# Optimization experiments

Hardware: AMD Instinct MI355X
Metric: run time of the kernel (lower is better)

The kernel has to match this reference:

```python
import jax, jax.numpy as jnp
import numpy as np

B, L, D_TOK, N_HEAD, D_QK, D_V, TOPK = 4, 1024, 897, 8, 512, 768, 8
NEG = -10000.0


def setup_inputs() -> dict:
    key = jax.random.key(0)
    ks = jax.random.split(key, 8)
    q = jax.random.normal(ks[0], (B, L, D_TOK), jnp.float32)
    k = jax.random.normal(ks[1], (B, L, D_TOK), jnp.float32)
    v = jax.random.normal(ks[2], (B, L, D_V), jnp.float32)
    # self-patch exclusion mask (registered buffer 10000*eye, applied negatively)
    qk_mask = NEG * jnp.eye(L, dtype=jnp.float32)[None, None]  # [1,1,L,L]
    k_mask = jax.random.normal(ks[3], (B, 1, L, 1), jnp.float32)  # additive key mask
    w_qs = jax.random.normal(ks[4], (D_TOK, N_HEAD * D_QK), jnp.float32) / np.sqrt(D_TOK)
    w_ks = jax.random.normal(ks[5], (D_TOK, N_HEAD * D_QK), jnp.float32) / np.sqrt(D_TOK)
    w_vs = jax.random.normal(ks[6], (D_V, N_HEAD * D_V), jnp.float32) / np.sqrt(D_V)
    w_fc = jax.random.normal(ks[7], (N_HEAD * D_V, D_V), jnp.float32) / np.sqrt(N_HEAD * D_V)
    return {"q": q, "k": k, "v": v, "qk_mask": qk_mask, "k_mask": k_mask,
            "w_qs": w_qs, "w_ks": w_ks, "w_vs": w_vs, "w_fc": w_fc}


def _topk_sparsify(attn):
    # keep top-k scores per query row, set the rest to -10000 (exact torch scatter semantics)
    vals, idx = jax.lax.top_k(attn, TOPK)                      # [B,H,L,TOPK]
    flat = jnp.full((B * N_HEAD * L, L), NEG, attn.dtype)
    rows = jnp.arange(B * N_HEAD * L)[:, None]
    flat = flat.at[rows, idx.reshape(-1, TOPK)].set(vals.reshape(-1, TOPK))
    return flat.reshape(B, N_HEAD, L, L)


def reference(q, k, v, qk_mask, k_mask, w_qs, w_ks, w_vs, w_fc):
    # projections -> [B, H, L, d]
    qh = (q @ w_qs).reshape(B, L, N_HEAD, D_QK).transpose(0, 2, 1, 3)
    kh = (k @ w_ks).reshape(B, L, N_HEAD, D_QK).transpose(0, 2, 1, 3)
    vh = (v @ w_vs).reshape(B, L, N_HEAD, D_V).transpose(0, 2, 1, 3)
    scale = 1.0 / jnp.sqrt(jnp.asarray(D_QK, qh.dtype))
    attn = jnp.einsum('bhqd,bhkd->bhqk', qh * scale, kh)
    attn = attn + qk_mask + k_mask[..., 0][:, :, None, :]      # k_mask.squeeze(-1).unsqueeze(-2)
    attn = _topk_sparsify(attn)
    attn = jax.nn.softmax(attn.astype(jnp.float32), axis=-1).astype(v.dtype)
    out = jnp.einsum('bhqk,bhkd->bhqd', attn, vh)              # [B,H,L,d_v]
    out = out.transpose(0, 2, 1, 3).reshape(B, L, N_HEAD * D_V)
    out = out @ w_fc                                           # [B,L,d_v]; add_residual=False, dropout eval
    return out, attn
```

## Files before the change

### kernel.cpp

```cpp
#include <hip/hip_runtime.h>
#include <math.h>

#define NB 4
#define NL 1024
#define NDT 897
#define NH 8
#define NDQ 512
#define NDV 768
#define NTOP 8
#define NCAND 16
#define KP 928
#define SCALE 0.044194173824159216

typedef unsigned short ushort_t;
typedef __attribute__((ext_vector_type(8))) short short8;
typedef __attribute__((ext_vector_type(4))) float f32x4;

static __device__ __forceinline__ ushort_t f2bf(float f) {
    unsigned u = __float_as_uint(f);
    unsigned r = (u + 0x7fffu + ((u >> 16) & 1u)) >> 16;
    return (ushort_t)r;
}
static __device__ __forceinline__ float bf2f(ushort_t u) {
    return __uint_as_float((unsigned)u << 16);
}
static __device__ __forceinline__ void split3(float x, ushort_t& b1, ushort_t& b2, ushort_t& b3) {
    b1 = f2bf(x);
    float r1 = x - bf2f(b1);
    b2 = f2bf(r1);
    float r2 = r1 - bf2f(b2);
    b3 = f2bf(r2);
}
static __device__ __forceinline__ void split2(float x, ushort_t& b1, ushort_t& b2) {
    b1 = f2bf(x);
    b2 = f2bf(x - bf2f(b1));
}

__global__ __launch_bounds__(256)
void split_w(const float* __restrict__ w_qs, const float* __restrict__ w_ks,
             ushort_t* __restrict__ wsp)
{
    const float* W = (blockIdx.z == 0) ? w_qs : w_ks;
    ushort_t* dst = wsp + (size_t)blockIdx.z * 3 * 4096 * KP;
    const int n0 = blockIdx.x * 64;
    const int k0 = blockIdx.y * 32;
    __shared__ float tf[32][65];
    const int t = threadIdx.x;
#pragma unroll
    for (int it = 0; it < 8; it++) {
        int kk = it * 4 + (t >> 6);
        int nn = t & 63;
        int kg = k0 + kk;
        tf[kk][nn] = (kg < NDT) ? W[(size_t)kg * 4096 + n0 + nn] : 0.f;
    }
    __syncthreads();
    const int nn = t >> 2;
    const int oct = t & 3;
    ushort_t o[3][8];
#pragma unroll
    for (int j = 0; j < 8; j++) {
        float x = tf[oct * 8 + j][nn];
        split3(x, o[0][j], o[1][j], o[2][j]);
    }
#pragma unroll
    for (int p = 0; p < 3; p++)
        *(uint4*)(dst + ((size_t)p * 4096 + n0 + nn) * KP + k0 + oct * 8) = *(const uint4*)o[p];
}

__global__ __launch_bounds__(256)
void split_wvs(const float* __restrict__ w_vs, ushort_t* __restrict__ wvs2)
{
    int gid8 = ((int)blockIdx.x * 256 + threadIdx.x) * 8;
    int dk  = gid8 / 6144;
    int rem = gid8 % 6144;
    int h   = rem / 768;
    int kk  = rem % 768;
    const float* src = w_vs + (size_t)dk * 6144 + rem;
    ushort_t o[2][8];
#pragma unroll
    for (int j = 0; j < 8; j++) split2(src[j], o[0][j], o[1][j]);
#pragma unroll
    for (int p = 0; p < 2; p++)
        *(uint4*)(wvs2 + ((size_t)(p * 8 + h) * 768 + dk) * 768 + kk) = *(const uint4*)o[p];
}

__global__ __launch_bounds__(256)
void split_wfcT(const float* __restrict__ w_fc, ushort_t* __restrict__ wfcT2)
{
    const int dv0 = blockIdx.x * 64;
    const int kg0 = blockIdx.y * 32;
    __shared__ float tf[32][65];
    const int t = threadIdx.x;
#pragma unroll
    for (int it = 0; it < 8; it++) {
        int kk = it * 4 + (t >> 6);
        int dd = t & 63;
        tf[kk][dd] = w_fc[(size_t)(kg0 + kk) * 768 + dv0 + dd];
    }
    __syncthreads();
    const int dv = t >> 2;
    const int oct = t & 3;
    const int h  = kg0 / 768;
    const int kl = kg0 % 768;
    ushort_t o[2][8];
#pragma unroll
    for (int j = 0; j < 8; j++) split2(tf[oct * 8 + j][dv], o[0][j], o[1][j]);
#pragma unroll
    for (int p = 0; p < 2; p++)
        *(uint4*)(wfcT2 + ((size_t)(p * 8 + h) * 768 + dv0 + dv) * 768 + kl + oct * 8) = *(const uint4*)o[p];
}

__global__ __launch_bounds__(256)
void combine_mfma(const ushort_t* __restrict__ wfcT2, const ushort_t* __restrict__ wvs2,
                  ushort_t* __restrict__ MhTb)
{
    const int h = blockIdx.z;
    const int n0 = blockIdx.x * 128, m0 = blockIdx.y * 128;
    __shared__ ushort_t Al[2 * 5120];
    __shared__ ushort_t Bl[2 * 5120];
    const int t = threadIdx.x;
    const int lane = t & 63, wv = t >> 6;
    const int quad = lane >> 4, l16 = lane & 15;

    f32x4 acc[2][8];
#pragma unroll
    for (int i = 0; i < 2; i++)
#pragma unroll
        for (int j = 0; j < 8; j++) acc[i][j] = (f32x4){0.f, 0.f, 0.f, 0.f};

    for (int kc = 0; kc < 768; kc += 32) {
#pragma unroll
        for (int p = 0; p < 2; p++) {
            const ushort_t* Ap = wfcT2 + (size_t)(p * 8 + h) * 768 * 768;
            const ushort_t* Bp = wvs2  + (size_t)(p * 8 + h) * 768 * 768;
#pragma unroll
            for (int pp = 0; pp < 2; pp++) {
                int c = t + pp * 256;
                int r = c >> 2, ck = c & 3;
                int pc = (ck + ((r + (r >> 3)) & 3)) & 3;
                uint4 va = *(const uint4*)(Ap + (size_t)(m0 + r) * 768 + kc + ck * 8);
                *(uint4*)&Al[p * 5120 + r * 40 + pc * 8] = va;
                uint4 vb = *(const uint4*)(Bp + (size_t)(n0 + r) * 768 + kc + ck * 8);
                *(uint4*)&Bl[p * 5120 + r * 40 + pc * 8] = vb;
            }
        }
        __syncthreads();

        short8 af[2][2], bf[2][8];
#pragma unroll
        for (int p = 0; p < 2; p++) {
#pragma unroll
            for (int i = 0; i < 2; i++) {
                int r = wv * 32 + i * 16 + l16;
                int pc = (quad + ((r + (r >> 3)) & 3)) & 3;
                af[p][i] = *(const short8*)&Al[p * 5120 + r * 40 + pc * 8];
            }
#pragma unroll
            for (int j = 0; j < 8; j++) {
                int r = j * 16 + l16;
                int pc = (quad + ((r + (r >> 3)) & 3)) & 3;
                bf[p][j] = *(const short8*)&Bl[p * 5120 + r * 40 + pc * 8];
            }
        }
#pragma unroll
        for (int i = 0; i < 2; i++)
#pragma unroll
            for (int j = 0; j < 8; j++) {
                acc[i][j] = __builtin_amdgcn_mfma_f32_16x16x32_bf16(af[0][i], bf[0][j], acc[i][j], 0, 0, 0);
                acc[i][j] = __builtin_amdgcn_mfma_f32_16x16x32_bf16(af[0][i], bf[1][j], acc[i][j], 0, 0, 0);
                acc[i][j] = __builtin_amdgcn_mfma_f32_16x16x32_bf16(af[1][i], bf[0][j], acc[i][j], 0, 0, 0);
            }
        __syncthreads();
    }

#pragma unroll
    for (int i = 0; i < 2; i++)
#pragma unroll
        for (int j = 0; j < 8; j++) {
            int gn = n0 + j * 16 + l16;
#pragma unroll
            for (int reg = 0; reg < 4; reg++) {
                int gm = m0 + wv * 32 + i * 16 + quad * 4 + reg;
                MhTb[((size_t)h * NDV + gm) * NDV + gn] = f2bf(acc[i][j][reg]);
            }
        }
}

__global__ __launch_bounds__(256)
void split_a(const float* __restrict__ q, const float* __restrict__ k,
             ushort_t* __restrict__ asp, int b)
{
    const int row = blockIdx.x;
    const int z = blockIdx.y;
    const float* A = (z == 0 ? q : k) + ((size_t)b * NL + row) * NDT;
    ushort_t* dst = asp + (size_t)z * 3 * 1024 * KP;
    const int t = threadIdx.x;
    if (t >= 232) return;
    const int kb = t * 4;
    ushort_t o[3][4];
#pragma unroll
    for (int j = 0; j < 4; j++) {
        int kk = kb + j;
        float x = (kk < NDT) ? A[kk] : 0.f;
        split3(x, o[0][j], o[1][j], o[2][j]);
    }
#pragma unroll
    for (int p = 0; p < 3; p++)
        *(uint2*)(dst + ((size_t)p * 1024 + row) * KP + kb) = *(const uint2*)o[p];
}

__global__ __launch_bounds__(256)
void proj_qk_mfma6(const ushort_t* __restrict__ asp, const ushort_t* __restrict__ wsp,
                   float* __restrict__ qh32, float* __restrict__ kh32,
                   ushort_t* __restrict__ qhb, ushort_t* __restrict__ khb)
{
    const int z = blockIdx.z;
    const int n0 = blockIdx.x * 128, m0 = blockIdx.y * 128;
    float*    C32 = z == 0 ? qh32 : kh32;
    ushort_t* Cb  = z == 0 ? qhb  : khb;
    const ushort_t* Ab = asp + (size_t)z * 3 * 1024 * KP;
    const ushort_t* Bb = wsp + (size_t)z * 3 * 4096 * KP;

    __shared__ ushort_t Al[3 * 128 * 40];
    __shared__ ushort_t Bl[3 * 128 * 40];
    const int t = threadIdx.x;
    const int lane = t & 63, wv = t >> 6;
    const int quad = lane >> 4, l16 = lane & 15;

    f32x4 acc[2][8];
#pragma unroll
    for (int i = 0; i < 2; i++)
#pragma unroll
        for (int j = 0; j < 8; j++) acc[i][j] = (f32x4){0.f, 0.f, 0.f, 0.f};

    for (int kc = 0; kc < KP; kc += 32) {
#pragma unroll
        for (int p = 0; p < 3; p++) {
            const ushort_t* Ap = Ab + (size_t)p * 1024 * KP;
            const ushort_t* Bp = Bb + (size_t)p * 4096 * KP;
#pragma unroll
            for (int pp = 0; pp < 2; pp++) {
                int c = t + pp * 256;
                int r = c >> 2, ck = c & 3;
                int pc = (ck + ((r + (r >> 3)) & 3)) & 3;
                uint4 va = *(const uint4*)(Ap + (size_t)(m0 + r) * KP + kc + ck * 8);
                *(uint4*)&Al[p * 5120 + r * 40 + pc * 8] = va;
                uint4 vb = *(const uint4*)(Bp + (size_t)(n0 + r) * KP + kc + ck * 8);
                *(uint4*)&Bl[p * 5120 + r * 40 + pc * 8] = vb;
            }
        }
        __syncthreads();

        short8 af[3][2], bf[3][8];
#pragma unroll
        for (int p = 0; p < 3; p++) {
#pragma unroll
            for (int i = 0; i < 2; i++) {
                int r = wv * 32 + i * 16 + l16;
                int pc = (quad + ((r + (r >> 3)) & 3)) & 3;
                af[p][i] = *(const short8*)&Al[p * 5120 + r * 40 + pc * 8];
            }
#pragma unroll
            for (int j = 0; j < 8; j++) {
                int r = j * 16 + l16;
                int pc = (quad + ((r + (r >> 3)) & 3)) & 3;
                bf[p][j] = *(const short8*)&Bl[p * 5120 + r * 40 + pc * 8];
            }
        }
#pragma unroll
        for (int i = 0; i < 2; i++)
#pragma unroll
            for (int j = 0; j < 8; j++) {
                acc[i][j] = __builtin_amdgcn_mfma_f32_16x16x32_bf16(af[0][i], bf[0][j], acc[i][j], 0, 0, 0);
                acc[i][j] = __builtin_amdgcn_mfma_f32_16x16x32_bf16(af[0][i], bf[1][j], acc[i][j], 0, 0, 0);
                acc[i][j] = __builtin_amdgcn_mfma_f32_16x16x32_bf16(af[1][i], bf[0][j], acc[i][j], 0, 0, 0);
                acc[i][j] = __builtin_amdgcn_mfma_f32_16x16x32_bf16(af[0][i], bf[2][j], acc[i][j], 0, 0, 0);
                acc[i][j] = __builtin_amdgcn_mfma_f32_16x16x32_bf16(af[1][i], bf[1][j], acc[i][j], 0, 0, 0);
                acc[i][j] = __builtin_amdgcn_mfma_f32_16x16x32_bf16(af[2][i], bf[0][j], acc[i][j], 0, 0, 0);
            }
        __syncthreads();
    }

#pragma unroll
    for (int i = 0; i < 2; i++)
#pragma unroll
        for (int j = 0; j < 8; j++) {
            int gn = n0 + j * 16 + l16;
#pragma unroll
            for (int reg = 0; reg < 4; reg++) {
                int gm = m0 + wv * 32 + i * 16 + quad * 4 + reg;
                float vv = acc[i][j][reg];
                C32[(size_t)gm * 4096 + gn] = vv;
                Cb[(size_t)gm * 4096 + gn] = f2bf(vv);
            }
        }
}

__global__ __launch_bounds__(256)
void scores_mfma(const ushort_t* __restrict__ qhb, const ushort_t* __restrict__ khb,
                 const float* __restrict__ kmask, float* __restrict__ sc, int b)
{
    const int h = blockIdx.z;
    const int n0 = blockIdx.x * 128, m0 = blockIdx.y * 128;
    __shared__ ushort_t Al[128 * 40];
    __shared__ ushort_t Bl[128 * 40];
    const int t = threadIdx.x;
    const int lane = t & 63, wv = t >> 6;
    const int quad = lane >> 4, l16 = lane & 15;

    f32x4 acc[2][8];
#pragma unroll
    for (int i = 0; i < 2; i++)
#pragma unroll
        for (int j = 0; j < 8; j++) acc[i][j] = (f32x4){0.f, 0.f, 0.f, 0.f};

    const ushort_t* Ag = qhb + (size_t)h * NDQ;
    const ushort_t* Bg = khb + (size_t)h * NDQ;

    for (int kc = 0; kc < NDQ; kc += 32) {
#pragma unroll
        for (int p = 0; p < 2; p++) {
            int c = t + p * 256;
            int r = c >> 2, ck = c & 3;
            int pc = (ck + ((r + (r >> 3)) & 3)) & 3;
            uint4 va = *(const uint4*)(Ag + (size_t)(m0 + r) * 4096 + kc + ck * 8);
            *(uint4*)&Al[r * 40 + pc * 8] = va;
        }
#pragma unroll
        for (int p = 0; p < 2; p++) {
            int c = t + p * 256;
            int r = c >> 2, ck = c & 3;
            int pc = (ck + ((r + (r >> 3)) & 3)) & 3;
            uint4 vb = *(const uint4*)(Bg + (size_t)(n0 + r) * 4096 + kc + ck * 8);
            *(uint4*)&Bl[r * 40 + pc * 8] = vb;
        }
        __syncthreads();

        short8 af[2], bf[8];
#pragma unroll
        for (int i = 0; i < 2; i++) {
            int r = wv * 32 + i * 16 + l16;
            int pc = (quad + ((r + (r >> 3)) & 3)) & 3;
            af[i] = *(const short8*)&Al[r * 40 + pc * 8];
        }
#pragma unroll
        for (int j = 0; j < 8; j++) {
            int r = j * 16 + l16;
            int pc = (quad + ((r + (r >> 3)) & 3)) & 3;
            bf[j] = *(const short8*)&Bl[r * 40 + pc * 8];
        }
#pragma unroll
        for (int i = 0; i < 2; i++)
#pragma unroll
            for (int j = 0; j < 8; j++)
                acc[i][j] = __builtin_amdgcn_mfma_f32_16x16x32_bf16(af[i], bf[j], acc[i][j], 0, 0, 0);
        __syncthreads();
    }

    const float scl = (float)SCALE;
#pragma unroll
    for (int i = 0; i < 2; i++) {
#pragma unroll
        for (int j = 0; j < 8; j++) {
            int gn = n0 + j * 16 + l16;
            float km = kmask[b * NL + gn];
#pragma unroll
            for (int reg = 0; reg < 4; reg++) {
                int gm = m0 + wv * 32 + i * 16 + quad * 4 + reg;
                float s = acc[i][j][reg] * scl + km;
                if (gm == gn) s -= 10000.0f;
                sc[((size_t)h * NL + gm) * NL + gn] = s;
            }
        }
    }
}

__global__ __launch_bounds__(256)
void select_rescore(float* __restrict__ sc,
                    const float* __restrict__ qh32, const float* __restrict__ kh32,
                    const float* __restrict__ kmask,
                    float* __restrict__ topw, int* __restrict__ topi, int b)
{
    const int lane = threadIdx.x & 63;
    const int w = threadIdx.x >> 6;
    const int r = blockIdx.x * 4 + w;
    const int q = r & 1023, h = r >> 10;

    float* row = sc + (size_t)r * NL;
    float v[16];
#pragma unroll
    for (int j = 0; j < 16; j++) v[j] = row[lane + 64 * j];

    {
        float4 z = make_float4(0.f, 0.f, 0.f, 0.f);
#pragma unroll
        for (int p = 0; p < 4; p++)
            *(float4*)(row + p * 256 + lane * 4) = z;
    }

    int cidx[NCAND];
    for (int tsel = 0; tsel < NCAND; tsel++) {
        float bv = v[0]; int bj = 0;
#pragma unroll
        for (int j = 1; j < 16; j++)
            if (v[j] > bv) { bv = v[j]; bj = j; }
        int bi = lane + 64 * bj;
#pragma unroll
        for (int s = 1; s < 64; s <<= 1) {
            float ov = __shfl_xor(bv, s);
            int   oi = __shfl_xor(bi, s);
            if (ov > bv || (ov == bv && oi < bi)) { bv = ov; bi = oi; }
        }
        cidx[tsel] = bi;
        bool own = (lane == (bi & 63));
        int jj = bi >> 6;
#pragma unroll
        for (int j = 0; j < 16; j++)
            if (own && j == jj) v[j] = -3.0e38f;
    }

    const float* qrow  = qh32 + (size_t)q * 4096 + h * NDQ;
    const float* kbase = kh32 + h * NDQ;
    double qd[8];
#pragma unroll
    for (int j = 0; j < 8; j++) qd[j] = (double)qrow[lane + 64 * j];

    double sv[NCAND]; int si[NCAND];
#pragma unroll
    for (int c = 0; c < NCAND; c++) {
        int idx = cidx[c];
        const float* krow = kbase + (size_t)idx * 4096;
        double s = 0.0;
#pragma unroll
        for (int j = 0; j < 8; j++) s = fma(qd[j], (double)krow[lane + 64 * j], s);
#pragma unroll
        for (int sh = 1; sh < 64; sh <<= 1) s += __shfl_xor(s, sh);
        s = s * SCALE + (double)kmask[b * NL + idx];
        if (idx == q) s -= 10000.0;
        sv[c] = s; si[c] = idx;
    }
    double vs[NTOP]; int is_[NTOP];
    unsigned used = 0;
#pragma unroll
    for (int tsel = 0; tsel < NTOP; tsel++) {
        double bv = -1.0e300; int bi = 1 << 30; int bc = 0;
#pragma unroll
        for (int c = 0; c < NCAND; c++) {
            bool free_c = !(used & (1u << c));
            bool better = free_c && (sv[c] > bv || (sv[c] == bv && si[c] < bi));
            if (better) { bv = sv[c]; bi = si[c]; bc = c; }
        }
        used |= (1u << bc);
        vs[tsel] = bv; is_[tsel] = bi;
    }
    double m = vs[0];
    double e[NTOP], Z = 0.0;
#pragma unroll
    for (int i = 0; i < NTOP; i++) { e[i] = exp(vs[i] - m); Z += e[i]; }

    __asm__ volatile("s_waitcnt vmcnt(0)" ::: "memory");

    if (lane == 0) {
#pragma unroll
        for (int i = 0; i < NTOP; i++) {
            float wv = (float)(e[i] / Z);
            topw[(size_t)r * NTOP + i] = wv;
            topi[(size_t)r * NTOP + i] = is_[i];
            row[is_[i]] = wv;
        }
    }
}

__global__ __launch_bounds__(256)
void conv_v_bf16(const float* __restrict__ v, ushort_t* __restrict__ vb)
{
    size_t i = ((size_t)blockIdx.x * 256 + threadIdx.x) * 4;
    float4 f = *(const float4*)(v + i);
    ushort_t o[4] = { f2bf(f.x), f2bf(f.y), f2bf(f.z), f2bf(f.w) };
    *(uint2*)(vb + i) = *(uint2*)o;
}

__global__ __launch_bounds__(256)
void vw_mfma(const ushort_t* __restrict__ vb, const ushort_t* __restrict__ MhTb,
             float* __restrict__ vw, int b)
{
    const int h = blockIdx.z;
    const int n0 = blockIdx.x * 128, m0 = blockIdx.y * 128;
    __shared__ ushort_t Al[128 * 40];
    __shared__ ushort_t Bl[128 * 40];
    const int t = threadIdx.x;
    const int lane = t & 63, wv = t >> 6;
    const int quad = lane >> 4, l16 = lane & 15;

    f32x4 acc[2][8];
#pragma unroll
    for (int i = 0; i < 2; i++)
#pragma unroll
        for (int j = 0; j < 8; j++) acc[i][j] = (f32x4){0.f, 0.f, 0.f, 0.f};

    const ushort_t* Ag = vb + (size_t)b * NL * NDV;
    const ushort_t* Bg = MhTb + (size_t)h * NDV * NDV;

    for (int kc = 0; kc < NDV; kc += 32) {
#pragma unroll
        for (int p = 0; p < 2; p++) {
            int c = t + p * 256;
            int r = c >> 2, ck = c & 3;
            int pc = (ck + ((r + (r >> 3)) & 3)) & 3;
            uint4 va = *(const uint4*)(Ag + (size_t)(m0 + r) * NDV + kc + ck * 8);
            *(uint4*)&Al[r * 40 + pc * 8] = va;
        }
#pragma unroll
        for (int p = 0; p < 2; p++) {
            int c = t + p * 256;
            int r = c >> 2, ck = c & 3;
            int pc = (ck + ((r + (r >> 3)) & 3)) & 3;
            uint4 vv = *(const uint4*)(Bg + (size_t)(n0 + r) * NDV + kc + ck * 8);
            *(uint4*)&Bl[r * 40 + pc * 8] = vv;
        }
        __syncthreads();

        short8 af[2], bf[8];
#pragma unroll
        for (int i = 0; i < 2; i++) {
            int r = wv * 32 + i * 16 + l16;
            int pc = (quad + ((r + (r >> 3)) & 3)) & 3;
            af[i] = *(const short8*)&Al[r * 40 + pc * 8];
        }
#pragma unroll
        for (int j = 0; j < 8; j++) {
            int r = j * 16 + l16;
            int pc = (quad + ((r + (r >> 3)) & 3)) & 3;
            bf[j] = *(const short8*)&Bl[r * 40 + pc * 8];
        }
#pragma unroll
        for (int i = 0; i < 2; i++)
#pragma unroll
            for (int j = 0; j < 8; j++)
                acc[i][j] = __builtin_amdgcn_mfma_f32_16x16x32_bf16(af[i], bf[j], acc[i][j], 0, 0, 0);
        __syncthreads();
    }

#pragma unroll
    for (int i = 0; i < 2; i++) {
#pragma unroll
        for (int j = 0; j < 8; j++) {
            int gn = n0 + j * 16 + l16;
#pragma unroll
            for (int reg = 0; reg < 4; reg++) {
                int gm = m0 + wv * 32 + i * 16 + quad * 4 + reg;
                vw[((size_t)h * NL + gm) * NDV + gn] = acc[i][j][reg];
            }
        }
    }
}

__global__ __launch_bounds__(256)
void gather_out(const float* __restrict__ vw, const float* __restrict__ topw,
                const int* __restrict__ topi, float* __restrict__ out, int b)
{
    const int q = blockIdx.x;
    __shared__ float sw[64];
    __shared__ int   sidx[64];
    const int t = threadIdx.x;
    if (t < 64) {
        int h = t >> 3, i = t & 7;
        size_t rr = ((size_t)h * NL + q) * NTOP + i;
        sw[t]   = topw[rr];
        sidx[t] = topi[rr] + h * NL;
    }
    __syncthreads();
    float* orow = out + (size_t)(b * NL + q) * NDV;
    for (int dv = t; dv < NDV; dv += 256) {
        float acc = 0.f;
#pragma unroll
        for (int j = 0; j < 64; j++)
            acc = fmaf(sw[j], vw[(size_t)sidx[j] * NDV + dv], acc);
        orow[dv] = acc;
    }
}

extern "C" void kernel_launch(void* const* d_in, const int* in_sizes, int n_in,
                              void* d_out, int out_size, void* d_ws, size_t ws_size,
                              hipStream_t stream)
{
    const float* q     = (const float*)d_in[0];
    const float* k     = (const float*)d_in[1];
    const float* v     = (const float*)d_in[2];
    const float* kmask = (const float*)d_in[4];
    const float* w_qs  = (const float*)d_in[5];
    const float* w_ks  = (const float*)d_in[6];
    const float* w_vs  = (const float*)d_in[7];
    const float* w_fc  = (const float*)d_in[8];

    char* ws = (char*)d_ws;
    float*    qh32 = (float*)   (ws + 0);
    float*    kh32 = (float*)   (ws + 16777216);
    ushort_t* qhb  = (ushort_t*)(ws + 33554432);
    ushort_t* khb  = (ushort_t*)(ws + 41943040);
    ushort_t* MhTb = (ushort_t*)(ws + 50331648);
    ushort_t* vb16 = (ushort_t*)(ws + 59768832);
    float*    topw = (float*)   (ws + 66060288);
    int*      topi = (int*)     (ws + 66322432);
    ushort_t* wsp  = (ushort_t*)(ws + 66584576);
    ushort_t* asp  = (ushort_t*)(ws + 112197632);
    float*    vw   = (float*)   (ws + 0);
    ushort_t* wfcT2 = (ushort_t*)(ws + 66584576);
    ushort_t* wvs2  = (ushort_t*)(ws + 66584576 + 18874368);

    float* out  = (float*)d_out;
    float* attn = out + (size_t)NB * NL * NDV;

    split_wvs   <<<2304, 256, 0, stream>>>(w_vs, wvs2);
    split_wfcT  <<<dim3(12, 192), 256, 0, stream>>>(w_fc, wfcT2);
    combine_mfma<<<dim3(6, 6, 8), 256, 0, stream>>>(wfcT2, wvs2, MhTb);
    split_w     <<<dim3(64, 29, 2), 256, 0, stream>>>(w_qs, w_ks, wsp);
    conv_v_bf16 <<<3072, 256, 0, stream>>>(v, vb16);

    for (int b = 0; b < NB; b++) {
        float* slab = attn + (size_t)b * NH * NL * NL;

        split_a       <<<dim3(1024, 2), 256, 0, stream>>>(q, k, asp, b);
        proj_qk_mfma6 <<<dim3(32, 8, 2), 256, 0, stream>>>(asp, wsp, qh32, kh32, qhb, khb);
        scores_mfma   <<<dim3(8, 8, 8), 256, 0, stream>>>(qhb, khb, kmask, slab, b);
        select_rescore<<<2048, 256, 0, stream>>>(slab, qh32, kh32, kmask, topw, topi, b);
        vw_mfma       <<<dim3(6, 8, 8), 256, 0, stream>>>(vb16, MhTb, vw, b);
        gather_out    <<<NL, 256, 0, stream>>>(vw, topw, topi, out, b);
    }
}
```

Baseline: 1.439 ms.

## Fuse per-tile top-16 candidate selection into scores GEMM epilogue

The scores kernel no longer writes the full fp32 score matrix. Each 128-column tile now selects its own top-16 candidates per row with in-register and shuffle reductions and writes them to a small candidate buffer. The rescore kernel reads 128 candidates per row instead of 1024 scores and no longer zeroes the row itself; the whole attention output is cleared once up front with a single memset. This cuts the score write and read traffic, at the cost of a serial 16-pass selection in the GEMM epilogue and a full-size memset.

```diff
diff --git a/kernel.cpp b/kernel.cpp
--- a/kernel.cpp
+++ b/kernel.cpp
@@ -297,11 +297,13 @@
 }
 
 __global__ __launch_bounds__(256)
-void scores_mfma(const ushort_t* __restrict__ qhb, const ushort_t* __restrict__ khb,
-                 const float* __restrict__ kmask, float* __restrict__ sc, int b)
+void scores_cand(const ushort_t* __restrict__ qhb, const ushort_t* __restrict__ khb,
+                 const float* __restrict__ kmask,
+                 float* __restrict__ candv, int* __restrict__ candi, int b)
 {
     const int h = blockIdx.z;
     const int n0 = blockIdx.x * 128, m0 = blockIdx.y * 128;
+    const int bx = blockIdx.x;
     __shared__ ushort_t Al[128 * 40];
     __shared__ ushort_t Bl[128 * 40];
     const int t = threadIdx.x;
@@ -359,7 +361,7 @@
 
     const float scl = (float)SCALE;
 #pragma unroll
-    for (int i = 0; i < 2; i++) {
+    for (int i = 0; i < 2; i++)
 #pragma unroll
         for (int j = 0; j < 8; j++) {
             int gn = n0 + j * 16 + l16;
@@ -369,16 +371,48 @@
                 int gm = m0 + wv * 32 + i * 16 + quad * 4 + reg;
                 float s = acc[i][j][reg] * scl + km;
                 if (gm == gn) s -= 10000.0f;
-                sc[((size_t)h * NL + gm) * NL + gn] = s;
-            }
-        }
-    }
-}
-
-__global__ __launch_bounds__(256)
-void select_rescore(float* __restrict__ sc,
+                acc[i][j][reg] = s;
+            }
+        }
+
+#pragma unroll
+    for (int slot = 0; slot < 8; slot++) {
+        const int i = slot >> 2, reg = slot & 3;
+        const int gr = m0 + wv * 32 + i * 16 + quad * 4 + reg;
+        float vv[8];
+#pragma unroll
+        for (int j = 0; j < 8; j++) vv[j] = acc[i][j][reg];
+        for (int it = 0; it < 16; it++) {
+            float bv = vv[0]; int bj = 0;
+#pragma unroll
+            for (int j = 1; j < 8; j++)
+                if (vv[j] > bv) { bv = vv[j]; bj = j; }
+            int bc = bj * 16 + l16;
+#pragma unroll
+            for (int s = 1; s < 16; s <<= 1) {
+                float ov = __shfl_xor(bv, s);
+                int   oc = __shfl_xor(bc, s);
+                if (ov > bv || (ov == bv && oc < bc)) { bv = ov; bc = oc; }
+            }
+            if (l16 == it) {
+                size_t o = (((size_t)h * NL + gr) * 8 + bx) * 16 + it;
+                candv[o] = bv;
+                candi[o] = n0 + bc;
+            }
+            int wj = bc >> 4, wl = bc & 15;
+            if (l16 == wl) {
+#pragma unroll
+                for (int j = 0; j < 8; j++)
+                    if (j == wj) vv[j] = -3.0e38f;
+            }
+        }
+    }
+}
+
+__global__ __launch_bounds__(256)
+void select_rescore(const float* __restrict__ candv, const int* __restrict__ candi,
                     const float* __restrict__ qh32, const float* __restrict__ kh32,
-                    const float* __restrict__ kmask,
+                    const float* __restrict__ kmask, float* __restrict__ attn,
                     float* __restrict__ topw, int* __restrict__ topi, int b)
 {
     const int lane = threadIdx.x & 63;
@@ -386,25 +420,17 @@
     const int r = blockIdx.x * 4 + w;
     const int q = r & 1023, h = r >> 10;
 
-    float* row = sc + (size_t)r * NL;
-    float v[16];
-#pragma unroll
-    for (int j = 0; j < 16; j++) v[j] = row[lane + 64 * j];
-
+    float cv[2]; int ci[2];
     {
-        float4 z = make_float4(0.f, 0.f, 0.f, 0.f);
-#pragma unroll
-        for (int p = 0; p < 4; p++)
-            *(float4*)(row + p * 256 + lane * 4) = z;
+        size_t base = (size_t)r * 128 + lane * 2;
+        cv[0] = candv[base];     cv[1] = candv[base + 1];
+        ci[0] = candi[base];     ci[1] = candi[base + 1];
     }
 
     int cidx[NCAND];
     for (int tsel = 0; tsel < NCAND; tsel++) {
-        float bv = v[0]; int bj = 0;
-#pragma unroll
-        for (int j = 1; j < 16; j++)
-            if (v[j] > bv) { bv = v[j]; bj = j; }
-        int bi = lane + 64 * bj;
+        float bv = cv[0]; int bi = ci[0];
+        if (cv[1] > bv || (cv[1] == bv && ci[1] < bi)) { bv = cv[1]; bi = ci[1]; }
 #pragma unroll
         for (int s = 1; s < 64; s <<= 1) {
             float ov = __shfl_xor(bv, s);
@@ -412,11 +438,8 @@
             if (ov > bv || (ov == bv && oi < bi)) { bv = ov; bi = oi; }
         }
         cidx[tsel] = bi;
-        bool own = (lane == (bi & 63));
-        int jj = bi >> 6;
-#pragma unroll
-        for (int j = 0; j < 16; j++)
-            if (own && j == jj) v[j] = -3.0e38f;
+        if (ci[0] == bi) cv[0] = -3.0e38f;
+        if (ci[1] == bi) cv[1] = -3.0e38f;
     }
 
     const float* qrow  = qh32 + (size_t)q * 4096 + h * NDQ;
@@ -458,9 +481,8 @@
 #pragma unroll
     for (int i = 0; i < NTOP; i++) { e[i] = exp(vs[i] - m); Z += e[i]; }
 
-    __asm__ volatile("s_waitcnt vmcnt(0)" ::: "memory");
-
     if (lane == 0) {
+        float* row = attn + (size_t)r * NL;
 #pragma unroll
         for (int i = 0; i < NTOP; i++) {
             float wv = (float)(e[i] / Z);
@@ -607,9 +629,13 @@
     float*    vw   = (float*)   (ws + 0);
     ushort_t* wfcT2 = (ushort_t*)(ws + 66584576);
     ushort_t* wvs2  = (ushort_t*)(ws + 66584576 + 18874368);
+    float* candv = (float*)(ws + 112197632);
+    int*   candi = (int*)  (ws + 116391936);
 
     float* out  = (float*)d_out;
     float* attn = out + (size_t)NB * NL * NDV;
+
+    hipMemsetAsync(attn, 0, (size_t)NB * NH * NL * NL * sizeof(float), stream);
 
     split_wvs   <<<2304, 256, 0, stream>>>(w_vs, wvs2);
     split_wfcT  <<<dim3(12, 192), 256, 0, stream>>>(w_fc, wfcT2);
@@ -622,8 +648,9 @@
 
         split_a       <<<dim3(1024, 2), 256, 0, stream>>>(q, k, asp, b);
         proj_qk_mfma6 <<<dim3(32, 8, 2), 256, 0, stream>>>(asp, wsp, qh32, kh32, qhb, khb);
-        scores_mfma   <<<dim3(8, 8, 8), 256, 0, stream>>>(qhb, khb, kmask, slab, b);
-        select_rescore<<<2048, 256, 0, stream>>>(slab, qh32, kh32, kmask, topw, topi, b);
+        scores_cand   <<<dim3(8, 8, 8), 256, 0, stream>>>(qhb, khb, kmask, candv, candi, b);
+        select_rescore<<<2048, 256, 0, stream>>>(candv, candi, qh32, kh32, kmask,
+                                                 slab, topw, topi, b);
         vw_mfma       <<<dim3(6, 8, 8), 256, 0, stream>>>(vb16, MhTb, vw, b);
         gather_out    <<<NL, 256, 0, stream>>>(vw, topw, topi, out, b);
     }
```

After: 1.687 ms. 17.2% more time.
